# Kernel tuning notes

Hardware: AMD Instinct MI355X
Metric: run time of the kernel (lower is better)

The kernel has to match this reference:

```python
import jax, jax.numpy as jnp
import numpy as np
from jax import lax

NEIGHBOR_KERNEL = jnp.array([[1.0, 1.0, 1.0],
                             [1.0, 0.0, 1.0],
                             [1.0, 1.0, 1.0]], dtype=jnp.float32).reshape(1, 1, 3, 3)  # OIHW


def setup_inputs() -> dict:
    key = jax.random.key(0)
    # Binary occupancy grid (cellular automaton state), 4096x4096 fp32
    x = jnp.round(jax.random.uniform(key, (4096, 4096), dtype=jnp.float32))
    return {"x": x, "convs": 32}


def reference(x, convs):
    y = x[None, None, :, :]  # (1,1,H,W) NCHW

    def body(i, y):
        # 3x3 neighbor sum (center excluded), 'same' zero padding
        sums = lax.conv_general_dilated(
            y, NEIGHBOR_KERNEL, window_strides=(1, 1), padding="SAME",
            dimension_numbers=("NCHW", "OIHW", "NCHW"))
        # keep cell only if it has more than 3 live neighbors
        return jnp.where(sums > 3.0, y, jnp.zeros_like(y))

    y = lax.fori_loop(0, convs, body, y)
    return jnp.sum(x) - jnp.sum(y)
```

## Files before the change

kernel.cpp:

```cpp
#include <hip/hip_runtime.h>
#include <cstdint>

#define GRID_N 4096
#define WPR 64
#define NROWS 4096
#define NWORDS (WPR * NROWS)

#define KF 16
#define OUT 16
#define SPAN (OUT + 2 * KF)
#define RPW (SPAN / 8)
#define NBLK (NROWS / OUT)
#define PACK_BLOCKS 2048

__global__ __launch_bounds__(256) void pack_kernel(const float* __restrict__ x,
                                                   uint64_t* __restrict__ bits,
                                                   unsigned long long* __restrict__ px) {
    int lane = threadIdx.x & 63;
    int wv = threadIdx.x >> 6;
    int gw = blockIdx.x * 4 + wv;
    unsigned long long pc = 0;
    #pragma unroll
    for (int it = 0; it < 8; ++it) {
        int c = gw * 8 + it;
        size_t base = (size_t)c * 256 + lane;
        uint64_t my = 0;
        #pragma unroll
        for (int j = 0; j < 4; ++j) {
            float v = x[base + (size_t)j * 64];
            uint64_t m = __ballot(v > 0.5f);
            if (lane == j) my = m;
        }
        if (lane < 4) {
            bits[(c << 2) + lane] = my;
            pc += (unsigned long long)__popcll(my);
        }
    }
    for (int off = 32; off; off >>= 1) pc += __shfl_down(pc, off, 64);
    __shared__ unsigned long long part[4];
    if (lane == 0) part[wv] = pc;
    __syncthreads();
    if (threadIdx.x == 0)
        px[blockIdx.x] = part[0] + part[1] + part[2] + part[3];
}

template <bool POP>
__global__ __launch_bounds__(512) void step_kernel(const uint64_t* __restrict__ in,
                                                   uint64_t* __restrict__ out,
                                                   unsigned long long* __restrict__ py) {
    const int lane = threadIdx.x & 63;
    const int wv = threadIdx.x >> 6;
    const int b = blockIdx.x;
    const int w4 = wv * RPW;
    const int gbase = b * OUT - KF;

    uint64_t r[RPW];
    #pragma unroll
    for (int i = 0; i < RPW; ++i) {
        int gr = gbase + w4 + i;
        r[i] = (gr >= 0 && gr < NROWS) ? in[(size_t)gr * WPR + lane] : 0ULL;
    }

    __shared__ uint64_t bnd[2][8][2][64];

    #pragma unroll 2
    for (int g = 1; g <= KF; ++g) {
        const int p = g & 1;
        bnd[p][wv][0][lane] = r[0];
        bnd[p][wv][1][lane] = r[RPW - 1];
        __syncthreads();
        uint64_t up = (wv > 0) ? bnd[p][wv - 1][1][lane] : 0ULL;
        uint64_t dn = (wv < 7) ? bnd[p][wv + 1][0][lane] : 0ULL;

        uint64_t sv[RPW], cv[RPW];
        #pragma unroll
        for (int i = 0; i < RPW; ++i) {
            uint64_t a = (i == 0) ? up : r[i - 1];
            uint64_t d = (i == RPW - 1) ? dn : r[i + 1];
            uint64_t m = r[i];
            uint64_t t = a ^ m;
            sv[i] = t ^ d;
            cv[i] = (a & m) | (d & t);
        }

        uint32_t msgL = 0, msgR = 0;
        #pragma unroll
        for (int i = 0; i < RPW; ++i) {
            msgL |= ((uint32_t)(sv[i] >> 63) & 1u) << (2 * i);
            msgL |= ((uint32_t)(cv[i] >> 63) & 1u) << (2 * i + 1);
            msgR |= ((uint32_t)sv[i] & 1u) << (2 * i);
            msgR |= ((uint32_t)cv[i] & 1u) << (2 * i + 1);
        }
        uint32_t fromL = __shfl_up(msgL, 1);
        uint32_t fromR = __shfl_down(msgR, 1);
        fromL = (lane == 0) ? 0u : fromL;
        fromR = (lane == 63) ? 0u : fromR;

        #pragma unroll
        for (int i = 0; i < RPW; ++i) {
            int sr = w4 + i;
            if (sr >= g && sr < SPAN - g) {
                uint64_t sL = (sv[i] << 1) | (uint64_t)((fromL >> (2 * i)) & 1u);
                uint64_t cL = (cv[i] << 1) | (uint64_t)((fromL >> (2 * i + 1)) & 1u);
                uint64_t sR = (sv[i] >> 1) | ((uint64_t)((fromR >> (2 * i)) & 1u) << 63);
                uint64_t cR = (cv[i] >> 1) | ((uint64_t)((fromR >> (2 * i + 1)) & 1u) << 63);
                uint64_t t0, t1, u0, u1;
                { uint64_t tt = sL ^ sv[i]; t0 = tt ^ sR; t1 = (sL & sv[i]) | (sR & tt); }
                { uint64_t tt = cL ^ cv[i]; u0 = tt ^ cR; u1 = (cL & cv[i]) | (cR & tt); }
                uint64_t pp = t1 ^ u0, q = t1 & u0;
                uint64_t pred = (q & u1) | ((q ^ u1) & (pp | t0));
                r[i] &= pred;
            }
        }
    }

    if (!POP) {
        #pragma unroll
        for (int i = 0; i < RPW; ++i) {
            int sr = w4 + i;
            if (sr >= KF && sr < SPAN - KF)
                out[(size_t)(b * OUT + sr - KF) * WPR + lane] = r[i];
        }
    } else {
        unsigned long long pc = 0;
        #pragma unroll
        for (int i = 0; i < RPW; ++i) {
            int sr = w4 + i;
            if (sr >= KF && sr < SPAN - KF)
                pc += (unsigned long long)__popcll(r[i]);
        }
        for (int off = 32; off; off >>= 1) pc += __shfl_down(pc, off, 64);
        __shared__ unsigned long long part[8];
        if (lane == 0) part[wv] = pc;
        __syncthreads();
        if (threadIdx.x == 0) {
            unsigned long long s = 0;
            #pragma unroll
            for (int i = 0; i < 8; ++i) s += part[i];
            py[b] = s;
        }
    }
}

__global__ __launch_bounds__(256) void finalize_kernel(const unsigned long long* __restrict__ px,
                                                       const unsigned long long* __restrict__ py,
                                                       float* __restrict__ out) {
    int t = threadIdx.x;
    long long v = 0;
    #pragma unroll
    for (int i = 0; i < PACK_BLOCKS / 256; ++i)
        v += (long long)px[t + i * 256];
    v -= (long long)py[t];
    for (int off = 32; off; off >>= 1) v += __shfl_down(v, off, 64);
    __shared__ long long part[4];
    if ((t & 63) == 0) part[t >> 6] = v;
    __syncthreads();
    if (t == 0) out[0] = (float)(part[0] + part[1] + part[2] + part[3]);
}

extern "C" void kernel_launch(void* const* d_in, const int* in_sizes, int n_in,
                              void* d_out, int out_size, void* d_ws, size_t ws_size,
                              hipStream_t stream) {
    const float* x = (const float*)d_in[0];
    float* out = (float*)d_out;

    uint8_t* ws = (uint8_t*)d_ws;
    uint64_t* buf0 = (uint64_t*)ws;
    uint64_t* buf1 = (uint64_t*)(ws + (size_t)NWORDS * 8);
    unsigned long long* px = (unsigned long long*)(ws + (size_t)2 * NWORDS * 8);
    unsigned long long* py = px + PACK_BLOCKS;

    pack_kernel<<<PACK_BLOCKS, 256, 0, stream>>>(x, buf0, px);
    step_kernel<false><<<NBLK, 512, 0, stream>>>(buf0, buf1, nullptr);
    step_kernel<true ><<<NBLK, 512, 0, stream>>>(buf1, nullptr, py);
    finalize_kernel<<<1, 256, 0, stream>>>(px, py, out);
}
```

Measured before the change: 65.74 us.

## Fuse both step passes and finalize into one cooperative kernel with grid sync

Merges the two step_kernel launches and finalize_kernel into a single cooperative launch that uses grid.sync() between rounds and before the final reduction. In round two each block keeps its own middle rows in registers and reloads only the halo rows from global memory. The aim is to remove launch gaps and per-kernel ramp-up and tail costs. In exchange it adds cooperative-launch overhead and two grid-wide barriers across 256 blocks.

```diff
diff --git a/kernel.cpp b/kernel.cpp
--- a/kernel.cpp
+++ b/kernel.cpp
@@ -1,5 +1,8 @@
 #include <hip/hip_runtime.h>
+#include <hip/hip_cooperative_groups.h>
 #include <cstdint>
+
+namespace cg = cooperative_groups;
 
 #define GRID_N 4096
 #define WPR 64
@@ -44,118 +47,130 @@
         px[blockIdx.x] = part[0] + part[1] + part[2] + part[3];
 }
 
-template <bool POP>
-__global__ __launch_bounds__(512) void step_kernel(const uint64_t* __restrict__ in,
-                                                   uint64_t* __restrict__ out,
-                                                   unsigned long long* __restrict__ py) {
+__global__ __launch_bounds__(512) void life_kernel(
+        const uint64_t* __restrict__ buf0, uint64_t* __restrict__ buf1,
+        const unsigned long long* __restrict__ px,
+        unsigned long long* __restrict__ py, float* __restrict__ out) {
+    cg::grid_group grid = cg::this_grid();
     const int lane = threadIdx.x & 63;
     const int wv = threadIdx.x >> 6;
     const int b = blockIdx.x;
     const int w4 = wv * RPW;
     const int gbase = b * OUT - KF;
 
+    __shared__ uint64_t bnd[2][8][2][64];
     uint64_t r[RPW];
-    #pragma unroll
-    for (int i = 0; i < RPW; ++i) {
-        int gr = gbase + w4 + i;
-        r[i] = (gr >= 0 && gr < NROWS) ? in[(size_t)gr * WPR + lane] : 0ULL;
-    }
 
-    __shared__ uint64_t bnd[2][8][2][64];
-
-    #pragma unroll 2
-    for (int g = 1; g <= KF; ++g) {
-        const int p = g & 1;
-        bnd[p][wv][0][lane] = r[0];
-        bnd[p][wv][1][lane] = r[RPW - 1];
-        __syncthreads();
-        uint64_t up = (wv > 0) ? bnd[p][wv - 1][1][lane] : 0ULL;
-        uint64_t dn = (wv < 7) ? bnd[p][wv + 1][0][lane] : 0ULL;
-
-        uint64_t sv[RPW], cv[RPW];
-        #pragma unroll
-        for (int i = 0; i < RPW; ++i) {
-            uint64_t a = (i == 0) ? up : r[i - 1];
-            uint64_t d = (i == RPW - 1) ? dn : r[i + 1];
-            uint64_t m = r[i];
-            uint64_t t = a ^ m;
-            sv[i] = t ^ d;
-            cv[i] = (a & m) | (d & t);
-        }
-
-        uint32_t msgL = 0, msgR = 0;
-        #pragma unroll
-        for (int i = 0; i < RPW; ++i) {
-            msgL |= ((uint32_t)(sv[i] >> 63) & 1u) << (2 * i);
-            msgL |= ((uint32_t)(cv[i] >> 63) & 1u) << (2 * i + 1);
-            msgR |= ((uint32_t)sv[i] & 1u) << (2 * i);
-            msgR |= ((uint32_t)cv[i] & 1u) << (2 * i + 1);
-        }
-        uint32_t fromL = __shfl_up(msgL, 1);
-        uint32_t fromR = __shfl_down(msgR, 1);
-        fromL = (lane == 0) ? 0u : fromL;
-        fromR = (lane == 63) ? 0u : fromR;
-
+    for (int round = 0; round < 2; ++round) {
+        const uint64_t* src = (round == 0) ? buf0 : buf1;
         #pragma unroll
         for (int i = 0; i < RPW; ++i) {
             int sr = w4 + i;
-            if (sr >= g && sr < SPAN - g) {
-                uint64_t sL = (sv[i] << 1) | (uint64_t)((fromL >> (2 * i)) & 1u);
-                uint64_t cL = (cv[i] << 1) | (uint64_t)((fromL >> (2 * i + 1)) & 1u);
-                uint64_t sR = (sv[i] >> 1) | ((uint64_t)((fromR >> (2 * i)) & 1u) << 63);
-                uint64_t cR = (cv[i] >> 1) | ((uint64_t)((fromR >> (2 * i + 1)) & 1u) << 63);
-                uint64_t t0, t1, u0, u1;
-                { uint64_t tt = sL ^ sv[i]; t0 = tt ^ sR; t1 = (sL & sv[i]) | (sR & tt); }
-                { uint64_t tt = cL ^ cv[i]; u0 = tt ^ cR; u1 = (cL & cv[i]) | (cR & tt); }
-                uint64_t pp = t1 ^ u0, q = t1 & u0;
-                uint64_t pred = (q & u1) | ((q ^ u1) & (pp | t0));
-                r[i] &= pred;
+            if (round == 0 || sr < KF || sr >= KF + OUT) {
+                int gr = gbase + sr;
+                r[i] = (gr >= 0 && gr < NROWS) ? src[(size_t)gr * WPR + lane]
+                                               : 0ULL;
             }
+        }
+
+        #pragma unroll 2
+        for (int g = 1; g <= KF; ++g) {
+            const int p = g & 1;
+            bnd[p][wv][0][lane] = r[0];
+            bnd[p][wv][1][lane] = r[RPW - 1];
+            __syncthreads();
+            uint64_t up = (wv > 0) ? bnd[p][wv - 1][1][lane] : 0ULL;
+            uint64_t dn = (wv < 7) ? bnd[p][wv + 1][0][lane] : 0ULL;
+
+            uint64_t sv[RPW], cv[RPW];
+            #pragma unroll
+            for (int i = 0; i < RPW; ++i) {
+                uint64_t a = (i == 0) ? up : r[i - 1];
+                uint64_t d = (i == RPW - 1) ? dn : r[i + 1];
+                uint64_t m = r[i];
+                uint64_t t = a ^ m;
+                sv[i] = t ^ d;
+                cv[i] = (a & m) | (d & t);
+            }
+
+            uint32_t msgL = 0, msgR = 0;
+            #pragma unroll
+            for (int i = 0; i < RPW; ++i) {
+                msgL |= ((uint32_t)(sv[i] >> 63) & 1u) << (2 * i);
+                msgL |= ((uint32_t)(cv[i] >> 63) & 1u) << (2 * i + 1);
+                msgR |= ((uint32_t)sv[i] & 1u) << (2 * i);
+                msgR |= ((uint32_t)cv[i] & 1u) << (2 * i + 1);
+            }
+            uint32_t fromL = __shfl_up(msgL, 1);
+            uint32_t fromR = __shfl_down(msgR, 1);
+            fromL = (lane == 0) ? 0u : fromL;
+            fromR = (lane == 63) ? 0u : fromR;
+
+            #pragma unroll
+            for (int i = 0; i < RPW; ++i) {
+                int sr = w4 + i;
+                if (sr >= g && sr < SPAN - g) {
+                    uint64_t sL = (sv[i] << 1) | (uint64_t)((fromL >> (2 * i)) & 1u);
+                    uint64_t cL = (cv[i] << 1) | (uint64_t)((fromL >> (2 * i + 1)) & 1u);
+                    uint64_t sR = (sv[i] >> 1) | ((uint64_t)((fromR >> (2 * i)) & 1u) << 63);
+                    uint64_t cR = (cv[i] >> 1) | ((uint64_t)((fromR >> (2 * i + 1)) & 1u) << 63);
+                    uint64_t t0, t1, u0, u1;
+                    { uint64_t tt = sL ^ sv[i]; t0 = tt ^ sR; t1 = (sL & sv[i]) | (sR & tt); }
+                    { uint64_t tt = cL ^ cv[i]; u0 = tt ^ cR; u1 = (cL & cv[i]) | (cR & tt); }
+                    uint64_t pp = t1 ^ u0, q = t1 & u0;
+                    uint64_t pred = (q & u1) | ((q ^ u1) & (pp | t0));
+                    r[i] &= pred;
+                }
+            }
+        }
+
+        if (round == 0) {
+            #pragma unroll
+            for (int i = 0; i < RPW; ++i) {
+                int sr = w4 + i;
+                if (sr >= KF && sr < SPAN - KF)
+                    buf1[(size_t)(b * OUT + sr - KF) * WPR + lane] = r[i];
+            }
+            grid.sync();
         }
     }
 
-    if (!POP) {
+    unsigned long long pc = 0;
+    #pragma unroll
+    for (int i = 0; i < RPW; ++i) {
+        int sr = w4 + i;
+        if (sr >= KF && sr < SPAN - KF)
+            pc += (unsigned long long)__popcll(r[i]);
+    }
+    for (int off = 32; off; off >>= 1) pc += __shfl_down(pc, off, 64);
+    __shared__ unsigned long long part[8];
+    if (lane == 0) part[wv] = pc;
+    __syncthreads();
+    if (threadIdx.x == 0) {
+        unsigned long long s = 0;
         #pragma unroll
-        for (int i = 0; i < RPW; ++i) {
-            int sr = w4 + i;
-            if (sr >= KF && sr < SPAN - KF)
-                out[(size_t)(b * OUT + sr - KF) * WPR + lane] = r[i];
-        }
-    } else {
-        unsigned long long pc = 0;
-        #pragma unroll
-        for (int i = 0; i < RPW; ++i) {
-            int sr = w4 + i;
-            if (sr >= KF && sr < SPAN - KF)
-                pc += (unsigned long long)__popcll(r[i]);
-        }
-        for (int off = 32; off; off >>= 1) pc += __shfl_down(pc, off, 64);
-        __shared__ unsigned long long part[8];
-        if (lane == 0) part[wv] = pc;
+        for (int i = 0; i < 8; ++i) s += part[i];
+        py[b] = s;
+    }
+
+    grid.sync();
+
+    if (b == 0) {
+        int t = threadIdx.x;
+        long long v = (long long)px[t] + (long long)px[t + 512] +
+                      (long long)px[t + 1024] + (long long)px[t + 1536];
+        if (t < NBLK) v -= (long long)py[t];
+        for (int off = 32; off; off >>= 1) v += __shfl_down(v, off, 64);
+        __shared__ long long fin[8];
+        if (lane == 0) fin[wv] = v;
         __syncthreads();
-        if (threadIdx.x == 0) {
-            unsigned long long s = 0;
+        if (t == 0) {
+            long long s = 0;
             #pragma unroll
-            for (int i = 0; i < 8; ++i) s += part[i];
-            py[b] = s;
+            for (int i = 0; i < 8; ++i) s += fin[i];
+            out[0] = (float)s;
         }
     }
-}
-
-__global__ __launch_bounds__(256) void finalize_kernel(const unsigned long long* __restrict__ px,
-                                                       const unsigned long long* __restrict__ py,
-                                                       float* __restrict__ out) {
-    int t = threadIdx.x;
-    long long v = 0;
-    #pragma unroll
-    for (int i = 0; i < PACK_BLOCKS / 256; ++i)
-        v += (long long)px[t + i * 256];
-    v -= (long long)py[t];
-    for (int off = 32; off; off >>= 1) v += __shfl_down(v, off, 64);
-    __shared__ long long part[4];
-    if ((t & 63) == 0) part[t >> 6] = v;
-    __syncthreads();
-    if (t == 0) out[0] = (float)(part[0] + part[1] + part[2] + part[3]);
 }
 
 extern "C" void kernel_launch(void* const* d_in, const int* in_sizes, int n_in,
@@ -171,7 +186,8 @@
     unsigned long long* py = px + PACK_BLOCKS;
 
     pack_kernel<<<PACK_BLOCKS, 256, 0, stream>>>(x, buf0, px);
-    step_kernel<false><<<NBLK, 512, 0, stream>>>(buf0, buf1, nullptr);
-    step_kernel<true ><<<NBLK, 512, 0, stream>>>(buf1, nullptr, py);
-    finalize_kernel<<<1, 256, 0, stream>>>(px, py, out);
+
+    void* args[] = { (void*)&buf0, (void*)&buf1, (void*)&px, (void*)&py, (void*)&out };
+    hipLaunchCooperativeKernel(reinterpret_cast<void*>(life_kernel),
+                               dim3(NBLK), dim3(512), args, 0, stream);
 }
```

Result: slower. 128.8 us (+95.8%).
